# Kernel optimization log

Measured on AMD Instinct MI355X. Metric: run time of the kernel, lower is better.

## Reference

```python
import jax, jax.numpy as jnp
from jax import lax
import numpy as np

NPOINT = 1024
RADIUS = 0.1
NSAMPLE = 32
BN_EPS = 1e-5


def _fps(xyz, npoint):
    # xyz: [B, N, 3]. Deterministic start at index 0 (torch uses randint seed).
    B, N, _ = xyz.shape

    def step(carry, _):
        dist, far = carry
        centroid = jnp.take_along_axis(xyz, far[:, None, None], axis=1)  # [B,1,3]
        d = jnp.sum((xyz - centroid) ** 2, axis=-1)                      # [B,N]
        dist = jnp.minimum(dist, d)
        nxt = jnp.argmax(dist, axis=-1).astype(jnp.int32)
        return (dist, nxt), far

    init = (jnp.full((B, N), 1e10, xyz.dtype), jnp.zeros((B,), jnp.int32))
    _, idx = lax.scan(step, init, None, length=npoint)
    return jnp.transpose(idx)  # [B, npoint]


def _sqdist(a, b):
    # a: [B,S,3], b: [B,N,3] -> [B,S,N]
    return (jnp.sum(a * a, -1)[:, :, None] + jnp.sum(b * b, -1)[:, None, :]
            - 2.0 * jnp.einsum('bsc,bnc->bsn', a, b))


def _gather(pts, idx):
    # pts: [B,N,C], idx: [B,...] int -> [B,...,C]
    B = pts.shape[0]
    flat = idx.reshape(B, -1)
    out = jnp.take_along_axis(pts, flat[..., None], axis=1)
    return out.reshape(idx.shape + (pts.shape[-1],))


def _ball_query(radius, nsample, xyz, new_xyz):
    B, N, _ = xyz.shape
    sq = _sqdist(new_xyz, xyz)                                        # [B,S,N]
    ar = jnp.arange(N, dtype=jnp.int32)[None, None, :]
    gi = jnp.where(sq > radius ** 2, N, ar)                           # out-of-ball -> N
    gi = jnp.sort(gi, axis=-1)[:, :, :nsample]                        # [B,S,K]
    first = gi[:, :, :1]
    return jnp.where(gi == N, first, gi)                              # pad with first


def _sa_forward(xyz, points, params):
    # torch layout in: xyz [B,3,N], points [B,D,N]
    xyz = jnp.transpose(xyz, (0, 2, 1))        # [B,N,3]
    points = jnp.transpose(points, (0, 2, 1))  # [B,N,D]
    fps_idx = lax.stop_gradient(_fps(xyz, NPOINT))          # [B,S]
    new_xyz = _gather(xyz, fps_idx)                          # [B,S,3]
    idx = _ball_query(RADIUS, NSAMPLE, xyz, new_xyz)         # [B,S,K]
    g_xyz = _gather(xyz, idx) - new_xyz[:, :, None, :]       # [B,S,K,3]
    g_pts = _gather(points, idx)                             # [B,S,K,D]
    x = jnp.concatenate([g_xyz, g_pts], axis=-1)             # [B,S,K,3+D]
    for (W, b, g, bt, m, v) in params:
        x = jnp.einsum('bskc,oc->bsko', x, W) + b            # 1x1 conv
        x = (x - m) * (g / jnp.sqrt(v + BN_EPS)) + bt        # eval-mode BN
        x = jax.nn.relu(x)
    feat = jnp.max(x, axis=2)                                # max over K -> [B,S,C']
    return jnp.transpose(feat, (0, 2, 1))                    # [B,C',S]


def setup_inputs() -> dict:
    key = jax.random.key(0)
    ks = jax.random.split(key, 16)
    B, N = 4, 8192
    d = {}
    d['xyz'] = jax.random.uniform(ks[0], (B, 3, N), jnp.float32)       # unit cube cloud
    d['points'] = jax.random.normal(ks[1], (B, 3, N), jnp.float32)     # e.g. normals
    dims = [(6, 64), (64, 64), (64, 128)]
    k = 2
    for li, (cin, cout) in enumerate(dims, start=1):
        d[f'w{li}'] = jax.random.normal(ks[k], (cout, cin), jnp.float32) * (1.0 / np.sqrt(cin)); k += 1
        d[f'b{li}'] = jnp.zeros((cout,), jnp.float32)
        d[f'g{li}'] = jnp.ones((cout,), jnp.float32)
        d[f't{li}'] = jnp.zeros((cout,), jnp.float32)
        d[f'm{li}'] = jax.random.normal(ks[k], (cout,), jnp.float32) * 0.01; k += 1
        d[f'v{li}'] = jnp.ones((cout,), jnp.float32)
    return d


def reference(xyz, points,
              w1, b1, g1, t1, m1, v1,
              w2, b2, g2, t2, m2, v2,
              w3, b3, g3, t3, m3, v3):
    params = [(w1, b1, g1, t1, m1, v1),
              (w2, b2, g2, t2, m2, v2),
              (w3, b3, g3, t3, m3, v3)]
    return _sa_forward(xyz, points, params)
```

## Files before the change

### kernel.cpp

```cpp
#include <hip/hip_runtime.h>
#include <math.h>

#define NPTS 8192
#define NPOINT 1024
#define NSAMPLE 32

typedef float v2f __attribute__((ext_vector_type(2)));

template <int CTRL>
__device__ __forceinline__ float dpp_fmax_step(float v) {
  int s = __builtin_amdgcn_update_dpp(0, __float_as_int(v), CTRL, 0xF, 0xF, true);
  return fmaxf(v, __int_as_float(s));
}

__global__ __launch_bounds__(256, 1) void fps_kernel(const float4* __restrict__ xyz4,
                                                     float* __restrict__ new_xyz) {
#pragma clang fp contract(off)
  const int b = blockIdx.x;
  const int tid = threadIdx.x;
  const float4* xp4 = xyz4 + (size_t)b * NPTS;
  v2f px2[16], py2[16], pz2[16], d2[16];
#pragma unroll
  for (int j = 0; j < 16; ++j) {
    int n0 = tid + 512 * j;
    float4 a = xp4[n0];
    float4 c2 = xp4[n0 + 256];
    px2[j] = (v2f){a.x, c2.x};
    py2[j] = (v2f){a.y, c2.y};
    pz2[j] = (v2f){a.z, c2.z};
    d2[j] = (v2f){1e10f, 1e10f};
  }
  __shared__ unsigned long long red[2][4];
  float* outp = new_xyz + (size_t)b * NPOINT * 3;
  float4 c0 = xp4[0];
  float cx = c0.x, cy = c0.y, cz = c0.z;
  if (tid == 0) { outp[0] = cx; outp[1] = cy; outp[2] = cz; }
  for (int s = 1; s < NPOINT; ++s) {
    const v2f cxx = (v2f){cx, cx};
    const v2f cyy = (v2f){cy, cy};
    const v2f czz = (v2f){cz, cz};
    v2f vm2 = (v2f){-1.0f, -1.0f};
#pragma unroll
    for (int j = 0; j < 16; ++j) {
      v2f dx = px2[j] - cxx;
      v2f dy = py2[j] - cyy;
      v2f dz = pz2[j] - czz;
      v2f xx = dx * dx;
      v2f yy = dy * dy;
      v2f zz = dz * dz;
      v2f d = (xx + yy) + zz;
      float dmx = fminf(d2[j].x, d.x);
      float dmy = fminf(d2[j].y, d.y);
      d2[j].x = dmx;
      d2[j].y = dmy;
      vm2.x = fmaxf(vm2.x, dmx);
      vm2.y = fmaxf(vm2.y, dmy);
    }
    float bv = fmaxf(vm2.x, vm2.y);
    float m = bv;
    m = dpp_fmax_step<0x111>(m);
    m = dpp_fmax_step<0x112>(m);
    m = dpp_fmax_step<0x114>(m);
    m = dpp_fmax_step<0x118>(m);
    m = dpp_fmax_step<0x142>(m);
    m = dpp_fmax_step<0x143>(m);
    float Mw = __int_as_float(__builtin_amdgcn_readlane(__float_as_int(m), 63));
    int fi = 32;
    if (bv == Mw) {
#pragma unroll
      for (int j = 15; j >= 0; --j) {
        if (d2[j].y == bv) fi = 2 * j + 1;
        if (d2[j].x == bv) fi = 2 * j;
      }
    }
    int bi = tid + (fi << 8);
    unsigned long long mask = __ballot(bv == Mw);
    int bi_w;
    if (__popcll(mask) == 1) {
      bi_w = __builtin_amdgcn_readlane(bi, (int)(__ffsll(mask) - 1));
    } else {
      bi_w = NPTS;
      unsigned long long mm = mask;
      while (mm) {
        int l = (int)(__ffsll(mm) - 1);
        int bb = __builtin_amdgcn_readlane(bi, l);
        bi_w = (bb < bi_w) ? bb : bi_w;
        mm &= (mm - 1);
      }
    }
    unsigned long long key =
        ((unsigned long long)__float_as_uint(Mw) << 32) |
        (unsigned)(8191 - bi_w);
    if ((tid & 63) == 0) red[s & 1][tid >> 6] = key;
    __syncthreads();
    unsigned long long k0 = red[s & 1][0];
    unsigned long long k1 = red[s & 1][1];
    unsigned long long kB = red[s & 1][2];
    unsigned long long k3 = red[s & 1][3];
    unsigned long long ka = (k0 > k1) ? k0 : k1;
    unsigned long long kb = (kB > k3) ? kB : k3;
    unsigned long long km = (ka > kb) ? ka : kb;
    int gi = 8191 - (int)(unsigned)(km & 0xFFFFFFFFull);
    int giu = __builtin_amdgcn_readfirstlane(gi);
    float4 cc = xp4[giu];
    cx = cc.x; cy = cc.y; cz = cc.z;
    if (tid == 0) { outp[3 * s] = cx; outp[3 * s + 1] = cy; outp[3 * s + 2] = cz; }
  }
}

__global__ __launch_bounds__(256) void setup_kernel(
    const float* __restrict__ xyz, const float* __restrict__ w3,
    const float* __restrict__ b1, const float* __restrict__ g1, const float* __restrict__ t1,
    const float* __restrict__ m1, const float* __restrict__ v1,
    const float* __restrict__ b2, const float* __restrict__ g2, const float* __restrict__ t2,
    const float* __restrict__ m2, const float* __restrict__ v2,
    const float* __restrict__ b3, const float* __restrict__ g3, const float* __restrict__ t3,
    const float* __restrict__ m3, const float* __restrict__ v3,
    float4* __restrict__ xyz4, float* __restrict__ w3t, float* __restrict__ scsh) {
  int tid = threadIdx.x;
  int p = blockIdx.x * 256 + tid;
  int bb = p >> 13, n = p & 8191;
  const float* src = xyz + (size_t)bb * 3 * NPTS;
  xyz4[p] = make_float4(src[n], src[NPTS + n], src[2 * NPTS + n], 0.f);
  if (blockIdx.x != 0) return;
  for (int i = tid; i < 8192; i += 256) {
    int o = i >> 6, c = i & 63;
    w3t[c * 128 + o] = w3[i];
  }
  if (tid < 64) {
    float s = g1[tid] / sqrtf(v1[tid] + 1e-5f);
    scsh[tid] = s;
    scsh[64 + tid] = (b1[tid] - m1[tid]) * s + t1[tid];
    float s2 = g2[tid] / sqrtf(v2[tid] + 1e-5f);
    scsh[128 + tid] = s2;
    scsh[192 + tid] = (b2[tid] - m2[tid]) * s2 + t2[tid];
  }
  if (tid < 128) {
    float s3 = g3[tid] / sqrtf(v3[tid] + 1e-5f);
    scsh[256 + tid] = s3;
    scsh[384 + tid] = (b3[tid] - m3[tid]) * s3 + t3[tid];
  }
}

__global__ __launch_bounds__(256, 2) void mlp_kernel(
    const float* __restrict__ xyz, const float* __restrict__ points,
    const float* __restrict__ new_xyz,
    const float* __restrict__ w1, const float* __restrict__ w2,
    const float* __restrict__ w3t, const float* __restrict__ scsh,
    float* __restrict__ out) {
  __shared__ float act[256 * 64];
  float4* act4 = (float4*)act;
  const int tid = threadIdx.x;
  const int wv = tid >> 6, lane = tid & 63;
  const int s0 = blockIdx.x * 8;
  const int b = s0 >> 10;
  const int g = tid >> 5;
  const int k = tid & 31;
  const int gc = s0 + g;
  const float* xp = xyz + (size_t)b * 3 * NPTS;
  const float* pp = points + (size_t)b * 3 * NPTS;

  int* slots = (int*)(act + wv * 4096);
  {
#pragma clang fp contract(off)
    for (int h = 0; h < 2; ++h) {
      const int hc = s0 + 2 * wv + h;
      const float* cp0 = new_xyz + (size_t)hc * 3;
      const float cx = cp0[0], cy = cp0[1], cz = cp0[2];
      const float asq = (cx * cx + cy * cy) + cz * cz;
      int cnt = 0;
      for (int base = 0; base < NPTS; base += 64) {
        int n = base + lane;
        float x = xp[n], y = xp[NPTS + n], z = xp[2 * NPTS + n];
        float bsq = (x * x + y * y) + z * z;
        float ab = (x * cx + y * cy) + z * cz;
        float sq = (asq + bsq) - 2.0f * ab;
        bool inc = !(sq > 0.01f);
        unsigned long long mk = __ballot(inc);
        int pos = cnt + (int)__popcll(mk & ((1ull << lane) - 1ull));
        if (inc && pos < NSAMPLE) slots[h * 32 + pos] = n;
        cnt += (int)__popcll(mk);
        if (cnt >= NSAMPLE) break;
      }
      if (lane < NSAMPLE) {
        int first = slots[h * 32];
        int v = (lane < cnt) ? slots[h * 32 + lane] : first;
        slots[h * 32 + lane] = v;
      }
    }
  }
  const int n = slots[(g & 1) * 32 + k];

  const float* cp = new_xyz + (size_t)gc * 3;
  float f0 = xp[n] - cp[0];
  float f1 = xp[NPTS + n] - cp[1];
  float f2 = xp[2 * NPTS + n] - cp[2];
  float f3 = pp[n];
  float f4 = pp[NPTS + n];
  float f5 = pp[2 * NPTS + n];
  const float* sc1 = scsh;        const float* sh1 = scsh + 64;
  const float* sc2 = scsh + 128;  const float* sh2 = scsh + 192;
  const float* sc3 = scsh + 256;  const float* sh3 = scsh + 384;
  const int row = tid;

#pragma unroll
  for (int oc = 0; oc < 16; ++oc) {
    float va[4];
#pragma unroll
    for (int jj = 0; jj < 4; ++jj) {
      int o = oc * 4 + jj;
      const float* wr = w1 + o * 6;
      float a = f0 * wr[0] + f1 * wr[1] + f2 * wr[2] +
                f3 * wr[3] + f4 * wr[4] + f5 * wr[5];
      va[jj] = fmaxf(a * sc1[o] + sh1[o], 0.f);
    }
    act4[row * 16 + (oc ^ (row & 15))] = make_float4(va[0], va[1], va[2], va[3]);
  }

  float acc[64];
#pragma unroll
  for (int o = 0; o < 64; ++o) acc[o] = 0.f;
  for (int cc = 0; cc < 16; ++cc) {
    float4 av = act4[row * 16 + (cc ^ (row & 15))];
#pragma unroll
    for (int o = 0; o < 64; ++o) {
      const float* wr = w2 + o * 64 + cc * 4;
      acc[o] += av.x * wr[0] + av.y * wr[1] + av.z * wr[2] + av.w * wr[3];
    }
  }
#pragma unroll
  for (int oc = 0; oc < 16; ++oc) {
    float va[4];
#pragma unroll
    for (int jj = 0; jj < 4; ++jj) {
      int o = oc * 4 + jj;
      va[jj] = fmaxf(acc[o] * sc2[o] + sh2[o], 0.f);
    }
    act4[row * 16 + (oc ^ (row & 15))] = make_float4(va[0], va[1], va[2], va[3]);
  }
  __syncthreads();

  const int j = k;
  const int sb = gc & 1023;
  for (int ph = 0; ph < 2; ++ph) {
    int o3a = ph * 64 + j;
    int o3b = o3a + 32;
    float wa[64], wb[64];
#pragma unroll
    for (int c = 0; c < 64; ++c) {
      wa[c] = w3t[c * 128 + o3a];
      wb[c] = w3t[c * 128 + o3b];
    }
    float sca = sc3[o3a], sha = sh3[o3a];
    float scb = sc3[o3b], shb = sh3[o3b];
    float vma = 0.f, vmb = 0.f;
    for (int kk = 0; kk < 32; ++kk) {
      int r2 = g * 32 + kk;
      float a0 = 0.f, a1 = 0.f, a2 = 0.f, a3 = 0.f;
      float b0 = 0.f, b1 = 0.f, b2 = 0.f, b3 = 0.f;
#pragma unroll
      for (int cc = 0; cc < 16; cc += 4) {
        float4 u0 = act4[r2 * 16 + ((cc + 0) ^ (r2 & 15))];
        float4 u1 = act4[r2 * 16 + ((cc + 1) ^ (r2 & 15))];
        float4 u2 = act4[r2 * 16 + ((cc + 2) ^ (r2 & 15))];
        float4 u3 = act4[r2 * 16 + ((cc + 3) ^ (r2 & 15))];
        a0 += u0.x * wa[4*cc+0]  + u0.y * wa[4*cc+1]  + u0.z * wa[4*cc+2]  + u0.w * wa[4*cc+3];
        a1 += u1.x * wa[4*cc+4]  + u1.y * wa[4*cc+5]  + u1.z * wa[4*cc+6]  + u1.w * wa[4*cc+7];
        a2 += u2.x * wa[4*cc+8]  + u2.y * wa[4*cc+9]  + u2.z * wa[4*cc+10] + u2.w * wa[4*cc+11];
        a3 += u3.x * wa[4*cc+12] + u3.y * wa[4*cc+13] + u3.z * wa[4*cc+14] + u3.w * wa[4*cc+15];
        b0 += u0.x * wb[4*cc+0]  + u0.y * wb[4*cc+1]  + u0.z * wb[4*cc+2]  + u0.w * wb[4*cc+3];
        b1 += u1.x * wb[4*cc+4]  + u1.y * wb[4*cc+5]  + u1.z * wb[4*cc+6]  + u1.w * wb[4*cc+7];
        b2 += u2.x * wb[4*cc+8]  + u2.y * wb[4*cc+9]  + u2.z * wb[4*cc+10] + u2.w * wb[4*cc+11];
        b3 += u3.x * wb[4*cc+12] + u3.y * wb[4*cc+13] + u3.z * wb[4*cc+14] + u3.w * wb[4*cc+15];
      }
      float xa = (a0 + a1) + (a2 + a3);
      float xb = (b0 + b1) + (b2 + b3);
      vma = fmaxf(vma, fmaxf(xa * sca + sha, 0.f));
      vmb = fmaxf(vmb, fmaxf(xb * scb + shb, 0.f));
    }
    out[((size_t)b * 128 + o3a) * 1024 + sb] = vma;
    out[((size_t)b * 128 + o3b) * 1024 + sb] = vmb;
  }
}

extern "C" void kernel_launch(void* const* d_in, const int* in_sizes, int n_in,
                              void* d_out, int out_size, void* d_ws, size_t ws_size,
                              hipStream_t stream) {
  (void)in_sizes; (void)n_in; (void)out_size; (void)ws_size;
  const float* xyz    = (const float*)d_in[0];
  const float* points = (const float*)d_in[1];
  const float* w1 = (const float*)d_in[2];
  const float* b1 = (const float*)d_in[3];
  const float* g1 = (const float*)d_in[4];
  const float* t1 = (const float*)d_in[5];
  const float* m1 = (const float*)d_in[6];
  const float* v1 = (const float*)d_in[7];
  const float* w2 = (const float*)d_in[8];
  const float* b2 = (const float*)d_in[9];
  const float* g2 = (const float*)d_in[10];
  const float* t2 = (const float*)d_in[11];
  const float* m2 = (const float*)d_in[12];
  const float* v2 = (const float*)d_in[13];
  const float* w3 = (const float*)d_in[14];
  const float* b3 = (const float*)d_in[15];
  const float* g3 = (const float*)d_in[16];
  const float* t3 = (const float*)d_in[17];
  const float* m3 = (const float*)d_in[18];
  const float* v3 = (const float*)d_in[19];

  float* wsf = (float*)d_ws;
  float* new_xyz = wsf;
  float* w3t     = wsf + 12288;
  float* scsh    = w3t + 8192;
  float4* xyz4   = (float4*)(scsh + 512);
  float* out     = (float*)d_out;

  hipLaunchKernelGGL(setup_kernel, dim3(128), dim3(256), 0, stream,
                     xyz, w3, b1, g1, t1, m1, v1, b2, g2, t2, m2, v2,
                     b3, g3, t3, m3, v3, xyz4, w3t, scsh);
  hipLaunchKernelGGL(fps_kernel, dim3(4), dim3(256), 0, stream, xyz4, new_xyz);
  hipLaunchKernelGGL(mlp_kernel, dim3(512), dim3(256), 0, stream,
                     xyz, points, new_xyz, w1, w2, w3t, scsh, out);
}
```

Before: 1.489 ms.

## Spatially sort points by Morton code and prune FPS slabs via bounding-box bounds

The setup kernel now sorts each batch's points by 30-bit Morton code with a shared-memory bitonic sort, writes sorted coordinates plus original indices, and computes a bounding box for each 32-point slab. The FPS kernel keeps all coordinates and running min-distances in LDS. Each iteration it skips slabs whose box lower bound cannot lower that slab's cached max distance, so only active slabs are updated. A per-slab 64-bit key (distance, original index, position) feeds a DPP and shared-memory argmax that keeps the original-index tie-break. This aims to cut the per-iteration distance work, but adds a serial bitonic sort on only 4 blocks, atomics, and extra barriers per iteration.

```diff
diff --git a/kernel.cpp b/kernel.cpp
--- a/kernel.cpp
+++ b/kernel.cpp
@@ -5,106 +5,134 @@
 #define NPOINT 1024
 #define NSAMPLE 32
 
-typedef float v2f __attribute__((ext_vector_type(2)));
-
 template <int CTRL>
-__device__ __forceinline__ float dpp_fmax_step(float v) {
-  int s = __builtin_amdgcn_update_dpp(0, __float_as_int(v), CTRL, 0xF, 0xF, true);
-  return fmaxf(v, __int_as_float(s));
-}
-
-__global__ __launch_bounds__(256, 1) void fps_kernel(const float4* __restrict__ xyz4,
-                                                     float* __restrict__ new_xyz) {
+__device__ __forceinline__ unsigned long long dpp_umax64(unsigned long long key) {
+  int lo = (int)(unsigned)key;
+  int hi = (int)(unsigned)(key >> 32);
+  int slo = __builtin_amdgcn_update_dpp(0, lo, CTRL, 0xF, 0xF, true);
+  int shi = __builtin_amdgcn_update_dpp(0, hi, CTRL, 0xF, 0xF, true);
+  unsigned long long o =
+      ((unsigned long long)(unsigned)shi << 32) | (unsigned)slo;
+  return (o > key) ? o : key;
+}
+
+__device__ __forceinline__ unsigned p1b2(unsigned v) {
+  v &= 0x3FFu;
+  v = (v | (v << 16)) & 0x030000FFu;
+  v = (v | (v << 8)) & 0x0300F00Fu;
+  v = (v | (v << 4)) & 0x030C30C3u;
+  v = (v | (v << 2)) & 0x09249249u;
+  return v;
+}
+
+__global__ __launch_bounds__(256, 1) void fps_kernel(
+    const float* __restrict__ xyz, const float4* __restrict__ coord4g,
+    const unsigned* __restrict__ io_g32, const float* __restrict__ anch_g,
+    float* __restrict__ new_xyz) {
 #pragma clang fp contract(off)
+  extern __shared__ char smem[];
+  float4* coord4 = (float4*)smem;
+  unsigned* ioL32 = (unsigned*)(smem + 131072);
+  const unsigned short* ioL16 = (const unsigned short*)(smem + 131072);
+  unsigned long long* ck = (unsigned long long*)(smem + 147456);
+  unsigned* list2 = (unsigned*)(smem + 149504);
+  unsigned long long* red = (unsigned long long*)(smem + 151552);
+  unsigned* lcnt = (unsigned*)(smem + 151616);
+
   const int b = blockIdx.x;
-  const int tid = threadIdx.x;
-  const float4* xp4 = xyz4 + (size_t)b * NPTS;
-  v2f px2[16], py2[16], pz2[16], d2[16];
-#pragma unroll
-  for (int j = 0; j < 16; ++j) {
-    int n0 = tid + 512 * j;
-    float4 a = xp4[n0];
-    float4 c2 = xp4[n0 + 256];
-    px2[j] = (v2f){a.x, c2.x};
-    py2[j] = (v2f){a.y, c2.y};
-    pz2[j] = (v2f){a.z, c2.z};
-    d2[j] = (v2f){1e10f, 1e10f};
-  }
-  __shared__ unsigned long long red[2][4];
+  const int t = threadIdx.x;
+  const float4* cg = coord4g + (size_t)b * NPTS;
+#pragma unroll
+  for (int m = 0; m < 32; ++m) {
+    int i = m * 256 + t;
+    float4 f = cg[i];
+    f.w = 1e10f;
+    coord4[i] = f;
+  }
+  const unsigned* iog = io_g32 + (size_t)b * 4096;
+#pragma unroll
+  for (int m = 0; m < 16; ++m) {
+    int i = m * 256 + t;
+    ioL32[i] = iog[i];
+  }
+  ck[t] = ((unsigned long long)0x7F800000u) << 26;
+  if (t < 2) lcnt[t] = 0;
+  const float* ag = anch_g + ((size_t)b * 256 + t) * 6;
+  const float ax = ag[0], ay = ag[1], az = ag[2];
+  const float hx = ag[3], hy = ag[4], hz = ag[5];
+  const float* xp0 = xyz + (size_t)b * 3 * NPTS;
+  float cx = xp0[0], cy = xp0[NPTS], cz = xp0[2 * NPTS];
   float* outp = new_xyz + (size_t)b * NPOINT * 3;
-  float4 c0 = xp4[0];
-  float cx = c0.x, cy = c0.y, cz = c0.z;
-  if (tid == 0) { outp[0] = cx; outp[1] = cy; outp[2] = cz; }
+  if (t == 0) { outp[0] = cx; outp[1] = cy; outp[2] = cz; }
+  __syncthreads();
+
   for (int s = 1; s < NPOINT; ++s) {
-    const v2f cxx = (v2f){cx, cx};
-    const v2f cyy = (v2f){cy, cy};
-    const v2f czz = (v2f){cz, cz};
-    v2f vm2 = (v2f){-1.0f, -1.0f};
-#pragma unroll
-    for (int j = 0; j < 16; ++j) {
-      v2f dx = px2[j] - cxx;
-      v2f dy = py2[j] - cyy;
-      v2f dz = pz2[j] - czz;
-      v2f xx = dx * dx;
-      v2f yy = dy * dy;
-      v2f zz = dz * dz;
-      v2f d = (xx + yy) + zz;
-      float dmx = fminf(d2[j].x, d.x);
-      float dmy = fminf(d2[j].y, d.y);
-      d2[j].x = dmx;
-      d2[j].y = dmy;
-      vm2.x = fmaxf(vm2.x, dmx);
-      vm2.y = fmaxf(vm2.y, dmy);
-    }
-    float bv = fmaxf(vm2.x, vm2.y);
-    float m = bv;
-    m = dpp_fmax_step<0x111>(m);
-    m = dpp_fmax_step<0x112>(m);
-    m = dpp_fmax_step<0x114>(m);
-    m = dpp_fmax_step<0x118>(m);
-    m = dpp_fmax_step<0x142>(m);
-    m = dpp_fmax_step<0x143>(m);
-    float Mw = __int_as_float(__builtin_amdgcn_readlane(__float_as_int(m), 63));
-    int fi = 32;
-    if (bv == Mw) {
-#pragma unroll
-      for (int j = 15; j >= 0; --j) {
-        if (d2[j].y == bv) fi = 2 * j + 1;
-        if (d2[j].x == bv) fi = 2 * j;
+    const int p = s & 1;
+    float tx = fmaxf(fabsf(cx - ax) - hx, 0.f);
+    float ty = fmaxf(fabsf(cy - ay) - hy, 0.f);
+    float tz = fmaxf(fabsf(cz - az) - hz, 0.f);
+    float L = (tx * tx + ty * ty) + tz * tz;
+    float ckv = __uint_as_float((unsigned)(ck[t] >> 26));
+    bool active = !(L * 0.9999f >= ckv);
+    if (active) {
+      unsigned pos = atomicAdd(&lcnt[p], 1u);
+      list2[p * 256 + pos] = (unsigned)t;
+    }
+    __syncthreads();
+    const unsigned A = lcnt[p];
+    if (t == 0) lcnt[1 - p] = 0;
+    for (unsigned c0 = 0; c0 < A; c0 += 64) {
+      unsigned ci = c0 + ((unsigned)t >> 2);
+      if (ci < A) {
+        unsigned slab = list2[p * 256 + ci];
+        unsigned pb = slab * 32 + ((unsigned)t & 3u) * 8u;
+        unsigned long long tk = 0ull;
+#pragma unroll
+        for (unsigned e = 0; e < 8; ++e) {
+          unsigned pt = pb + e;
+          float4 f = coord4[pt];
+          float dx = f.x - cx;
+          float dy = f.y - cy;
+          float dz = f.z - cz;
+          float d = (dx * dx + dy * dy) + dz * dz;
+          float dm = fminf(f.w, d);
+          ((float*)&coord4[pt])[3] = dm;
+          unsigned orig = (unsigned)ioL16[pt];
+          unsigned long long kk =
+              ((unsigned long long)__float_as_uint(dm) << 26) |
+              ((unsigned long long)(8191u - orig) << 13) | pt;
+          tk = (kk > tk) ? kk : tk;
+        }
+        tk = dpp_umax64<0xB1>(tk);
+        tk = dpp_umax64<0x4E>(tk);
+        if (((unsigned)t & 3u) == 3u) ck[slab] = tk;
       }
     }
-    int bi = tid + (fi << 8);
-    unsigned long long mask = __ballot(bv == Mw);
-    int bi_w;
-    if (__popcll(mask) == 1) {
-      bi_w = __builtin_amdgcn_readlane(bi, (int)(__ffsll(mask) - 1));
-    } else {
-      bi_w = NPTS;
-      unsigned long long mm = mask;
-      while (mm) {
-        int l = (int)(__ffsll(mm) - 1);
-        int bb = __builtin_amdgcn_readlane(bi, l);
-        bi_w = (bb < bi_w) ? bb : bi_w;
-        mm &= (mm - 1);
-      }
-    }
-    unsigned long long key =
-        ((unsigned long long)__float_as_uint(Mw) << 32) |
-        (unsigned)(8191 - bi_w);
-    if ((tid & 63) == 0) red[s & 1][tid >> 6] = key;
     __syncthreads();
-    unsigned long long k0 = red[s & 1][0];
-    unsigned long long k1 = red[s & 1][1];
-    unsigned long long kB = red[s & 1][2];
-    unsigned long long k3 = red[s & 1][3];
+    unsigned long long kk = ck[t];
+    kk = dpp_umax64<0x111>(kk);
+    kk = dpp_umax64<0x112>(kk);
+    kk = dpp_umax64<0x114>(kk);
+    kk = dpp_umax64<0x118>(kk);
+    kk = dpp_umax64<0x142>(kk);
+    kk = dpp_umax64<0x143>(kk);
+    unsigned wlo = (unsigned)__builtin_amdgcn_readlane((int)(unsigned)kk, 63);
+    unsigned whi =
+        (unsigned)__builtin_amdgcn_readlane((int)(unsigned)(kk >> 32), 63);
+    if ((t & 63) == 0)
+      red[p * 4 + (t >> 6)] = ((unsigned long long)whi << 32) | wlo;
+    __syncthreads();
+    unsigned long long k0 = red[p * 4 + 0];
+    unsigned long long k1 = red[p * 4 + 1];
+    unsigned long long k2 = red[p * 4 + 2];
+    unsigned long long k3 = red[p * 4 + 3];
     unsigned long long ka = (k0 > k1) ? k0 : k1;
-    unsigned long long kb = (kB > k3) ? kB : k3;
+    unsigned long long kb = (k2 > k3) ? k2 : k3;
     unsigned long long km = (ka > kb) ? ka : kb;
-    int gi = 8191 - (int)(unsigned)(km & 0xFFFFFFFFull);
-    int giu = __builtin_amdgcn_readfirstlane(gi);
-    float4 cc = xp4[giu];
-    cx = cc.x; cy = cc.y; cz = cc.z;
-    if (tid == 0) { outp[3 * s] = cx; outp[3 * s + 1] = cy; outp[3 * s + 2] = cz; }
+    unsigned ptw = (unsigned)(km & 8191ull);
+    float4 cw = coord4[ptw];
+    cx = cw.x; cy = cw.y; cz = cw.z;
+    if (t == 0) { outp[3 * s] = cx; outp[3 * s + 1] = cy; outp[3 * s + 2] = cz; }
   }
 }
 
@@ -116,29 +144,82 @@
     const float* __restrict__ m2, const float* __restrict__ v2,
     const float* __restrict__ b3, const float* __restrict__ g3, const float* __restrict__ t3,
     const float* __restrict__ m3, const float* __restrict__ v3,
-    float4* __restrict__ xyz4, float* __restrict__ w3t, float* __restrict__ scsh) {
-  int tid = threadIdx.x;
-  int p = blockIdx.x * 256 + tid;
-  int bb = p >> 13, n = p & 8191;
-  const float* src = xyz + (size_t)bb * 3 * NPTS;
-  xyz4[p] = make_float4(src[n], src[NPTS + n], src[2 * NPTS + n], 0.f);
-  if (blockIdx.x != 0) return;
-  for (int i = tid; i < 8192; i += 256) {
+    float4* __restrict__ coord4g, unsigned short* __restrict__ io_g,
+    float* __restrict__ anch_g, float* __restrict__ w3t, float* __restrict__ scsh) {
+  __shared__ unsigned long long skey[NPTS];
+  const int b = blockIdx.x;
+  const int t = threadIdx.x;
+  const float* xp = xyz + (size_t)b * 3 * NPTS;
+#pragma unroll
+  for (int m = 0; m < 32; ++m) {
+    int i = m * 256 + t;
+    float x = xp[i], y = xp[NPTS + i], z = xp[2 * NPTS + i];
+    unsigned xi = (unsigned)fminf(fmaxf(x, 0.f) * 1024.f, 1023.f);
+    unsigned yi = (unsigned)fminf(fmaxf(y, 0.f) * 1024.f, 1023.f);
+    unsigned zi = (unsigned)fminf(fmaxf(z, 0.f) * 1024.f, 1023.f);
+    unsigned long long mort =
+        ((unsigned long long)p1b2(zi) << 2) |
+        ((unsigned long long)p1b2(yi) << 1) | (unsigned long long)p1b2(xi);
+    skey[i] = (mort << 13) | (unsigned)i;
+  }
+  __syncthreads();
+  for (int k = 2; k <= NPTS; k <<= 1) {
+    for (int j = k >> 1; j > 0; j >>= 1) {
+      for (int m = 0; m < 32; ++m) {
+        int i = m * 256 + t;
+        int ixj = i ^ j;
+        if (ixj > i) {
+          unsigned long long a = skey[i], c = skey[ixj];
+          bool up = ((i & k) == 0);
+          if ((a > c) == up) { skey[i] = c; skey[ixj] = a; }
+        }
+      }
+      __syncthreads();
+    }
+  }
+#pragma unroll
+  for (int m = 0; m < 32; ++m) {
+    int i = m * 256 + t;
+    unsigned orig = (unsigned)(skey[i] & 8191ull);
+    float x = xp[orig], y = xp[NPTS + orig], z = xp[2 * NPTS + orig];
+    coord4g[(size_t)b * NPTS + i] = make_float4(x, y, z, 0.f);
+    io_g[(size_t)b * NPTS + i] = (unsigned short)orig;
+  }
+  __syncthreads();
+  {
+    float mnx = 1e30f, mny = 1e30f, mnz = 1e30f;
+    float mxx = -1e30f, mxy = -1e30f, mxz = -1e30f;
+    for (int e = 0; e < 32; ++e) {
+      float4 f = coord4g[(size_t)b * NPTS + t * 32 + e];
+      mnx = fminf(mnx, f.x); mxx = fmaxf(mxx, f.x);
+      mny = fminf(mny, f.y); mxy = fmaxf(mxy, f.y);
+      mnz = fminf(mnz, f.z); mxz = fmaxf(mxz, f.z);
+    }
+    float cax = 0.5f * (mnx + mxx), cay = 0.5f * (mny + mxy), caz = 0.5f * (mnz + mxz);
+    float chx = fmaxf(mxx - cax, cax - mnx) * 1.000002f;
+    float chy = fmaxf(mxy - cay, cay - mny) * 1.000002f;
+    float chz = fmaxf(mxz - caz, caz - mnz) * 1.000002f;
+    float* agp = anch_g + ((size_t)b * 256 + t) * 6;
+    agp[0] = cax; agp[1] = cay; agp[2] = caz;
+    agp[3] = chx; agp[4] = chy; agp[5] = chz;
+  }
+  if (b != 0) return;
+  for (int i = t; i < 8192; i += 256) {
     int o = i >> 6, c = i & 63;
     w3t[c * 128 + o] = w3[i];
   }
-  if (tid < 64) {
-    float s = g1[tid] / sqrtf(v1[tid] + 1e-5f);
-    scsh[tid] = s;
-    scsh[64 + tid] = (b1[tid] - m1[tid]) * s + t1[tid];
-    float s2 = g2[tid] / sqrtf(v2[tid] + 1e-5f);
-    scsh[128 + tid] = s2;
-    scsh[192 + tid] = (b2[tid] - m2[tid]) * s2 + t2[tid];
-  }
-  if (tid < 128) {
-    float s3 = g3[tid] / sqrtf(v3[tid] + 1e-5f);
-    scsh[256 + tid] = s3;
-    scsh[384 + tid] = (b3[tid] - m3[tid]) * s3 + t3[tid];
+  if (t < 64) {
+    float s = g1[t] / sqrtf(v1[t] + 1e-5f);
+    scsh[t] = s;
+    scsh[64 + t] = (b1[t] - m1[t]) * s + t1[t];
+    float s2 = g2[t] / sqrtf(v2[t] + 1e-5f);
+    scsh[128 + t] = s2;
+    scsh[192 + t] = (b2[t] - m2[t]) * s2 + t2[t];
+  }
+  if (t < 128) {
+    float s3 = g3[t] / sqrtf(v3[t] + 1e-5f);
+    scsh[256 + t] = s3;
+    scsh[384 + t] = (b3[t] - m3[t]) * s3 + t3[t];
   }
 }
 
@@ -311,14 +392,20 @@
   float* wsf = (float*)d_ws;
   float* new_xyz = wsf;
   float* w3t     = wsf + 12288;
-  float* scsh    = w3t + 8192;
-  float4* xyz4   = (float4*)(scsh + 512);
+  float* scsh    = wsf + 20480;
+  float4* coord4g = (float4*)(wsf + 20992);
+  unsigned short* io_g = (unsigned short*)(wsf + 152064);
+  float* anch_g  = wsf + 168448;
   float* out     = (float*)d_out;
 
-  hipLaunchKernelGGL(setup_kernel, dim3(128), dim3(256), 0, stream,
+  hipFuncSetAttribute(reinterpret_cast<const void*>(fps_kernel),
+                      hipFuncAttributeMaxDynamicSharedMemorySize, 151680);
+
+  hipLaunchKernelGGL(setup_kernel, dim3(4), dim3(256), 0, stream,
                      xyz, w3, b1, g1, t1, m1, v1, b2, g2, t2, m2, v2,
-                     b3, g3, t3, m3, v3, xyz4, w3t, scsh);
-  hipLaunchKernelGGL(fps_kernel, dim3(4), dim3(256), 0, stream, xyz4, new_xyz);
+                     b3, g3, t3, m3, v3, coord4g, io_g, anch_g, w3t, scsh);
+  hipLaunchKernelGGL(fps_kernel, dim3(4), dim3(256), 151680, stream,
+                     xyz, coord4g, (const unsigned*)io_g, anch_g, new_xyz);
   hipLaunchKernelGGL(mlp_kernel, dim3(512), dim3(256), 0, stream,
                      xyz, points, new_xyz, w1, w2, w3t, scsh, out);
 }
```

Result: slower. 1.857 ms (+24.8%).
